# Optimization experiments

Measured on AMD Instinct MI355X. Metric: run time of the kernel, lower is better.

The kernel has to match this reference:

```python
import jax, jax.numpy as jnp
import numpy as np

JOINTS = 17
SKELETON = ((1, 2), (0, 1), (0, 2), (2, 4), (1, 3), (6, 8), (8, 10), (5, 7), (7, 9),
            (12, 14), (14, 16), (11, 13), (13, 15), (5, 6), (11, 12), (5, 11), (6, 12),
            (3, 5), (4, 6))
DIM = 512
HEADS = 8
HEAD_DIM = DIM // HEADS
SCALE = HEAD_DIM ** -0.5
ON = 64           # obj_emb seq len; HEADS*ON must equal 512 (size of W)
HIDDEN = 4 * DIM
BN_EPS = 1e-5
LN_EPS = 1e-5


def make_adj():
    a = np.eye(JOINTS, dtype=np.float32)
    for i, j in SKELETON:
        a[i, j] = 1.0
        a[j, i] = 1.0
    return jnp.asarray(a)


def layer_norm(x, w, b):
    mu = jnp.mean(x, axis=-1, keepdims=True)
    var = jnp.var(x, axis=-1, keepdims=True)
    return (x - mu) * jax.lax.rsqrt(var + LN_EPS) * w + b


def setup_inputs() -> dict:
    key = jax.random.key(0)
    ks = jax.random.split(key, 12)
    B = 2048
    inp = {
        "noise": jax.random.normal(ks[0], (B, JOINTS, DIM), jnp.float32),
        "obj_emb": jax.random.normal(ks[1], (B, ON, DIM), jnp.float32),
        "ln1_w": jnp.ones((DIM,), jnp.float32),
        "ln1_b": jnp.zeros((DIM,), jnp.float32),
        "ln2_w": jnp.ones((DIM,), jnp.float32),
        "ln2_b": jnp.zeros((DIM,), jnp.float32),
        "q_w": jax.random.normal(ks[2], (DIM, DIM), jnp.float32) * 0.02,
        "kv_w": jax.random.normal(ks[3], (2 * DIM, DIM), jnp.float32) * 0.02,
        "W": jax.random.normal(ks[4], (HEADS * ON, HEADS * ON), jnp.float32) * 0.001,
        "bn_g": jnp.ones((HEADS * ON,), jnp.float32),
        "bn_b": jnp.zeros((HEADS * ON,), jnp.float32),
        "proj_w": jax.random.normal(ks[5], (DIM, DIM), jnp.float32) * 0.02,
        "proj_b": jnp.zeros((DIM,), jnp.float32),
        "fc1_w": jax.random.normal(ks[6], (HIDDEN, DIM), jnp.float32) * 0.02,
        "fc1_b": jnp.zeros((HIDDEN,), jnp.float32),
        "fc2_w": jax.random.normal(ks[7], (DIM, HIDDEN), jnp.float32) * 0.02,
        "fc2_b": jnp.zeros((DIM,), jnp.float32),
    }
    return inp


def reference(noise, obj_emb, ln1_w, ln1_b, ln2_w, ln2_b, q_w, kv_w, W,
              bn_g, bn_b, proj_w, proj_b, fc1_w, fc1_b, fc2_w, fc2_b):
    B = noise.shape[0]
    adj = make_adj()

    # --- attention branch (norm1 applied to both inputs with same params) ---
    x1 = layer_norm(noise, ln1_w, ln1_b)          # [B,17,C]
    e1 = layer_norm(obj_emb, ln1_w, ln1_b)        # [B,64,C]

    q = (x1 @ q_w.T).reshape(B, JOINTS, HEADS, HEAD_DIM).transpose(0, 2, 1, 3)  # [B,H,17,hd]
    kv = (e1 @ kv_w.T).reshape(B, ON, 2, HEADS, HEAD_DIM).transpose(2, 0, 3, 1, 4)
    k, v = kv[0], kv[1]                            # [B,H,64,hd]

    attn = jnp.einsum('bhnd,bhmd->bhnm', q, k) * SCALE        # [B,H,17,64]
    attn = attn.transpose(0, 2, 1, 3).reshape(B, JOINTS, HEADS * ON)  # [B,17,512]
    attn = attn @ W                                            # [B,17,512]

    # BatchNorm1d (training mode): stats over B*17 rows, biased variance
    flat = attn.reshape(B * JOINTS, HEADS * ON)
    mu = jnp.mean(flat, axis=0)
    var = jnp.var(flat, axis=0)
    flat = (flat - mu) * jax.lax.rsqrt(var + BN_EPS) * bn_g + bn_b
    attn = flat.reshape(B, JOINTS, HEADS * ON)

    attn = jnp.einsum('ij,bjk->bik', adj, attn)               # adjacency bmm
    attn = attn.reshape(B, JOINTS, HEADS, ON).transpose(0, 2, 1, 3)  # [B,H,17,64]
    attn = jax.nn.softmax(attn, axis=-1)

    x = jnp.einsum('bhnm,bhmd->bhnd', attn, v)                # [B,H,17,hd]
    x = x.transpose(0, 2, 1, 3).reshape(B, JOINTS, DIM)
    x = x @ proj_w.T + proj_b

    x = noise + x

    # --- MLP branch ---
    y = layer_norm(x, ln2_w, ln2_b)
    y = jax.nn.gelu(y @ fc1_w.T + fc1_b, approximate=False)
    y = y @ fc2_w.T + fc2_b
    return x + y
```

## Files before the change

kernel.cpp:

```cpp
#include <hip/hip_runtime.h>
#include <math.h>

typedef unsigned short ushort_t;
typedef short short8 __attribute__((ext_vector_type(8)));
typedef float f32x4 __attribute__((ext_vector_type(4)));

#define MFMA16(a,b,c) __builtin_amdgcn_mfma_f32_16x16x32_bf16(a,b,c,0,0,0)

__device__ __forceinline__ ushort_t f2bf(float f){
  unsigned u = __builtin_bit_cast(unsigned, f);
  u += 0x7fffu + ((u >> 16) & 1u);
  return (ushort_t)(u >> 16);
}

__device__ __forceinline__ void gld16(const void* g, void* l){
  __builtin_amdgcn_global_load_lds(
      (const __attribute__((address_space(1))) void*)g,
      (__attribute__((address_space(3))) void*)l, 16, 0, 0);
}

__global__ __launch_bounds__(256)
void prep_weights(const float* __restrict__ q_w, const float* __restrict__ kv_w,
                  const float* __restrict__ proj_w, const float* __restrict__ fc1_w,
                  const float* __restrict__ fc2_w, const float* __restrict__ Wm,
                  const float* __restrict__ ln1w, const float* __restrict__ ln2w,
                  ushort_t* __restrict__ q_wb, ushort_t* __restrict__ kv_wb,
                  ushort_t* __restrict__ proj_wb, ushort_t* __restrict__ fc1_wb,
                  ushort_t* __restrict__ fc2_wb, ushort_t* __restrict__ Wt_b)
{
  int i = blockIdx.x*256 + threadIdx.x;
  if (i < 262144){
    q_wb[i] = f2bf(q_w[i] * ln1w[i & 511]);
  } else if (i < 786432){
    int j = i - 262144;
    kv_wb[j] = f2bf(kv_w[j] * ln1w[j & 511]);
  } else if (i < 1048576){
    int j = i - 786432;
    proj_wb[j] = f2bf(proj_w[j]);
  } else if (i < 2097152){
    int j = i - 1048576;
    fc1_wb[j] = f2bf(fc1_w[j] * ln2w[j & 511]);
  } else if (i < 3145728){
    int j = i - 2097152;
    fc2_wb[j] = f2bf(fc2_w[j]);
  } else if (i < 3407872){
    int j = i - 3145728;
    int n = j >> 9, k = j & 511;
    Wt_b[j] = f2bf(Wm[(k << 9) + n]);
  }
}

__global__ __launch_bounds__(64)
void prep_bias(const float* __restrict__ q_w, const float* __restrict__ kv_w,
               const float* __restrict__ fc1_w, const float* __restrict__ ln1b,
               const float* __restrict__ ln2b, const float* __restrict__ fc1_b,
               float* __restrict__ qbias, float* __restrict__ kvbias,
               float* __restrict__ fc1bias)
{
  int blk = blockIdx.x, lane = threadIdx.x;
  const float* w; const float* lnb; float* o; float base = 0.f; int n;
  if (blk < 512){ n = blk; w = q_w; lnb = ln1b; o = qbias; }
  else if (blk < 1536){ n = blk - 512; w = kv_w; lnb = ln1b; o = kvbias; }
  else { n = blk - 1536; w = fc1_w; lnb = ln2b; o = fc1bias; }
  float s = 0.f;
  for (int k = lane; k < 512; k += 64) s += w[(size_t)n*512 + k]*lnb[k];
  for (int m = 32; m; m >>= 1) s += __shfl_xor(s, m);
  if (lane == 0){
    if (blk >= 1536) base = fc1_b[n];
    o[n] = s + base;
  }
}

__global__ __launch_bounds__(256)
void lnorm(const float* __restrict__ X, ushort_t* __restrict__ O){
  int row = blockIdx.x*4 + (threadIdx.x >> 6);
  int lane = threadIdx.x & 63;
  const float4* p = (const float4*)(X + (size_t)row*512 + lane*8);
  float4 a = p[0], c = p[1];
  float s = a.x+a.y+a.z+a.w + c.x+c.y+c.z+c.w;
  float q = a.x*a.x+a.y*a.y+a.z*a.z+a.w*a.w + c.x*c.x+c.y*c.y+c.z*c.z+c.w*c.w;
  for (int m = 32; m; m >>= 1){ s += __shfl_xor(s, m); q += __shfl_xor(q, m); }
  float mn = s*(1.f/512.f);
  float rs = rsqrtf(q*(1.f/512.f) - mn*mn + 1e-5f);
  short8 pk;
  pk[0]=(short)f2bf((a.x-mn)*rs); pk[1]=(short)f2bf((a.y-mn)*rs);
  pk[2]=(short)f2bf((a.z-mn)*rs); pk[3]=(short)f2bf((a.w-mn)*rs);
  pk[4]=(short)f2bf((c.x-mn)*rs); pk[5]=(short)f2bf((c.y-mn)*rs);
  pk[6]=(short)f2bf((c.z-mn)*rs); pk[7]=(short)f2bf((c.w-mn)*rs);
  *(short8*)(O + (size_t)row*512 + lane*8) = pk;
}

template<int EPI>
__global__ __launch_bounds__(256, 3)
void gemm128(const ushort_t* __restrict__ A, const ushort_t* __restrict__ Bt,
             int M, int N, int K,
             const float* __restrict__ bias, const float* __restrict__ resid,
             void* __restrict__ out, void* __restrict__ out2)
{
  constexpr int ASLOT = 128*32;
  constexpr int SLOT  = 2*ASLOT;
  __shared__ __align__(16) ushort_t lds[3*SLOT];

  const int tid  = threadIdx.x;
  const int wave = tid >> 6, lane = tid & 63;
  const int wm   = wave >> 1, wn = wave & 1;
  const int l15  = lane & 15, lq = lane >> 4;

  const int nwg = gridDim.x;
  const int qc = nwg >> 3, rc = nwg & 7;
  const int xcd = blockIdx.x & 7, sl = blockIdx.x >> 3;
  const int bid = (xcd < rc ? xcd*(qc+1) : rc*(qc+1) + (xcd-rc)*qc) + sl;

  const int tiles_n = N >> 7;
  const int tn = bid % tiles_n, tm = bid / tiles_n;
  const int tileM = tm*128, tileN = tn*128;

  const int r0   = tid >> 2;
  const int r1   = (tid + 256) >> 2;
  const int g0   = (((tid & 3) - (r0 >> 1)) & 3) * 8;
  const int g1   = (((tid & 3) - (r1 >> 1)) & 3) * 8;
  const ushort_t* Ag0 = A  + (size_t)(tileM + r0)*K + g0;
  const ushort_t* Ag1 = A  + (size_t)(tileM + r1)*K + g1;
  const ushort_t* Bg0 = Bt + (size_t)(tileN + r0)*K + g0;
  const ushort_t* Bg1 = Bt + (size_t)(tileN + r1)*K + g1;

  auto stage = [&](int step, int slot){
    ushort_t* base = lds + slot*SLOT;
    const int k0 = step*32;
    gld16(Ag0 + k0, base + tid*8);
    gld16(Ag1 + k0, base + tid*8 + 2048);
    gld16(Bg0 + k0, base + ASLOT + tid*8);
    gld16(Bg1 + k0, base + ASLOT + tid*8 + 2048);
  };

  int offA[4], offB[4];
#pragma unroll
  for (int mi = 0; mi < 4; mi++){
    int r = wm*64 + mi*16 + l15;
    offA[mi] = r*32 + (((lq + (r >> 1)) & 3) * 8);
  }
#pragma unroll
  for (int ni = 0; ni < 4; ni++){
    int r = wn*64 + ni*16 + l15;
    offB[ni] = ASLOT + r*32 + (((lq + (r >> 1)) & 3) * 8);
  }

  f32x4 acc[4][4] = {};

  const int NT = K >> 5;

  stage(0, 0);
  stage(1, 1);
  asm volatile("s_waitcnt vmcnt(4)" ::: "memory");
  __builtin_amdgcn_sched_barrier(0);
  __builtin_amdgcn_s_barrier();
  __builtin_amdgcn_sched_barrier(0);

  int rs = 0;
  for (int s = 0; s < NT; ++s){
    const ushort_t* sb = lds + rs*SLOT;
    short8 aR[4], bR[4];
#pragma unroll
    for (int mi = 0; mi < 4; mi++) aR[mi] = *(const short8*)(sb + offA[mi]);
#pragma unroll
    for (int ni = 0; ni < 4; ni++) bR[ni] = *(const short8*)(sb + offB[ni]);

    const bool more = (s + 2 < NT);
    if (more){
      int r2 = rs + 2; if (r2 >= 3) r2 -= 3;
      stage(s + 2, r2);
    }

    __builtin_amdgcn_s_setprio(1);
#pragma unroll
    for (int mi = 0; mi < 4; mi++)
#pragma unroll
      for (int ni = 0; ni < 4; ni++)
        acc[mi][ni] = MFMA16(aR[mi], bR[ni], acc[mi][ni]);
    __builtin_amdgcn_s_setprio(0);

    if (more){
      asm volatile("s_waitcnt vmcnt(4)" ::: "memory");
    } else {
      asm volatile("s_waitcnt vmcnt(0)" ::: "memory");
    }
    __builtin_amdgcn_sched_barrier(0);
    __builtin_amdgcn_s_barrier();
    __builtin_amdgcn_sched_barrier(0);

    rs = (rs == 2) ? 0 : rs + 1;
  }

#pragma unroll
  for (int ni = 0; ni < 4; ni++){
    int col = tileN + wn*64 + ni*16 + l15;
    float bv = bias ? bias[col] : 0.f;
    float cs = 0.f, cq = 0.f;
#pragma unroll
    for (int mi = 0; mi < 4; mi++){
      f32x4 v = acc[mi][ni];
      int row0 = tileM + wm*64 + mi*16 + lq*4;
      if constexpr (EPI == 4){
        if (col < 512){
          for (int j = 0; j < 4; j++){
            size_t idx = (size_t)(row0 + j)*512 + col;
            ((ushort_t*)out)[idx] = f2bf(v[j] + bv);
          }
        } else {
          int hh = (col - 512) >> 6, dd = (col - 512) & 63;
          int bb2 = row0 >> 6, mm0 = row0 & 63;
          ushort_t pk[4];
          for (int j = 0; j < 4; j++) pk[j] = f2bf(v[j] + bv);
          *(uint2*)((ushort_t*)out2 + ((((size_t)bb2*8 + hh)*64 + dd) << 6) + mm0) =
              *(const uint2*)pk;
        }
      } else {
        for (int j = 0; j < 4; j++){
          int row = row0 + j;
          size_t idx = (size_t)row*N + col;
          float x = v[j] + bv;
          if constexpr (EPI == 0) ((ushort_t*)out)[idx] = f2bf(x);
          else if constexpr (EPI == 1) ((float*)out)[idx] = x;
          else if constexpr (EPI == 2) ((float*)out)[idx] = x + resid[idx];
          else if constexpr (EPI == 3){
            float g = 0.5f*x*(1.f + erff(x*0.70710678118f));
            ((ushort_t*)out)[idx] = f2bf(g);
          }
          else if constexpr (EPI == 5){
            ((float*)out)[idx] = x;
            cs += x; cq += x*x;
          }
        }
      }
    }
    if constexpr (EPI == 5){
      cs += __shfl_xor(cs, 16); cs += __shfl_xor(cs, 32);
      cq += __shfl_xor(cq, 16); cq += __shfl_xor(cq, 32);
      if (lq == 0){
        float* sums = (float*)out2;
        atomicAdd(&sums[col], cs);
        atomicAdd(&sums[512 + col], cq);
      }
    }
  }
}

__global__ __launch_bounds__(256)
void qk_kernel(const ushort_t* __restrict__ Q, const ushort_t* __restrict__ Kb,
               ushort_t* __restrict__ S)
{
  int b = blockIdx.x;
  int wave = threadIdx.x >> 6, lane = threadIdx.x & 63;
  for (int h = wave; h < 8; h += 4){
    f32x4 acc[2][4] = {};
    for (int kk = 0; kk < 2; kk++){
      int kd = kk*32 + (lane >> 4)*8;
      short8 a[2], bb[4];
      for (int mi = 0; mi < 2; mi++){
        int n = mi*16 + (lane & 15); if (n > 16) n = 16;
        a[mi] = *(const short8*)&Q[((size_t)b*17 + n)*512 + h*64 + kd];
      }
      for (int ni = 0; ni < 4; ni++){
        int m = ni*16 + (lane & 15);
        bb[ni] = *(const short8*)&Kb[((size_t)b*64 + m)*512 + h*64 + kd];
      }
      for (int mi = 0; mi < 2; mi++)
        for (int ni = 0; ni < 4; ni++)
          acc[mi][ni] = MFMA16(a[mi], bb[ni], acc[mi][ni]);
    }
    for (int mi = 0; mi < 2; mi++)
      for (int ni = 0; ni < 4; ni++)
        for (int j = 0; j < 4; j++){
          int rr = mi*16 + (lane >> 4)*4 + j;
          if (rr < 17)
            S[((size_t)b*17 + rr)*512 + h*64 + ni*16 + (lane & 15)] =
                f2bf(acc[mi][ni][j]*0.125f);
        }
  }
}

__global__ __launch_bounds__(256)
void pv_kernel(const ushort_t* __restrict__ P, const ushort_t* __restrict__ Vt,
               ushort_t* __restrict__ X)
{
  int b = blockIdx.x;
  int wave = threadIdx.x >> 6, lane = threadIdx.x & 63;
  for (int h = wave; h < 8; h += 4){
    f32x4 acc[2][4] = {};
    for (int kk = 0; kk < 2; kk++){
      int km = kk*32 + (lane >> 4)*8;
      short8 a[2], bb[4];
      for (int mi = 0; mi < 2; mi++){
        int n = mi*16 + (lane & 15); if (n > 16) n = 16;
        a[mi] = *(const short8*)&P[((size_t)b*17 + n)*512 + h*64 + km];
      }
      for (int ni = 0; ni < 4; ni++){
        int d = ni*16 + (lane & 15);
        bb[ni] = *(const short8*)&Vt[(((size_t)b*8 + h)*64 + d)*64 + km];
      }
      for (int mi = 0; mi < 2; mi++)
        for (int ni = 0; ni < 4; ni++)
          acc[mi][ni] = MFMA16(a[mi], bb[ni], acc[mi][ni]);
    }
    for (int mi = 0; mi < 2; mi++)
      for (int ni = 0; ni < 4; ni++)
        for (int j = 0; j < 4; j++){
          int rr = mi*16 + (lane >> 4)*4 + j;
          if (rr < 17)
            X[((size_t)b*17 + rr)*512 + h*64 + ni*16 + (lane & 15)] =
                f2bf(acc[mi][ni][j]);
        }
  }
}

__global__ void bn_finalize(const float* __restrict__ sums, const float* __restrict__ g,
                            const float* __restrict__ b, float* __restrict__ scale,
                            float* __restrict__ shift, float invN){
  int c = blockIdx.x*256 + threadIdx.x;
  if (c < 512){
    float mean = sums[c]*invN;
    float var  = sums[512 + c]*invN - mean*mean;
    float sc = g[c]*rsqrtf(var + 1e-5f);
    scale[c] = sc; shift[c] = b[c] - mean*sc;
  }
}

__constant__ unsigned ADJM[17] = {
  0x7u, 0xFu, 0x17u, 0x2Au, 0x54u, 0x8E8u, 0x1170u, 0x2A0u, 0x540u,
  0x280u, 0x500u, 0x3820u, 0x5840u, 0xA800u, 0x15000u, 0xA000u, 0x14000u };

__global__ __launch_bounds__(256)
void bn_adj_softmax(const float* __restrict__ preBN, const float* __restrict__ scale,
                    const float* __restrict__ shift, ushort_t* __restrict__ Asm)
{
  __shared__ float yt[17*512];
  int b = blockIdx.x, tid = threadIdx.x;
  const float* src = preBN + (size_t)b*17*512;
  for (int i = tid; i < 17*512; i += 256){
    int c = i & 511;
    yt[i] = src[i]*scale[c] + shift[c];
  }
  __syncthreads();
  int qw = tid >> 4, l16 = tid & 15;
  for (int g = qw; g < 136; g += 16){
    int n = g >> 3, h = g & 7;
    float z[4];
    unsigned msk = ADJM[n];
    for (int u = 0; u < 4; u++){
      int c = h*64 + l16 + u*16;
      float sv = 0.f;
      unsigned mm = msk;
      while (mm){ int j = __ffs(mm) - 1; mm &= mm - 1; sv += yt[j*512 + c]; }
      z[u] = sv;
    }
    float mx = fmaxf(fmaxf(z[0], z[1]), fmaxf(z[2], z[3]));
    for (int m = 8; m; m >>= 1) mx = fmaxf(mx, __shfl_xor(mx, m, 16));
    float e0 = expf(z[0]-mx), e1 = expf(z[1]-mx), e2 = expf(z[2]-mx), e3 = expf(z[3]-mx);
    float ss = e0 + e1 + e2 + e3;
    for (int m = 8; m; m >>= 1) ss += __shfl_xor(ss, m, 16);
    float inv = 1.f/ss;
    size_t ob = ((size_t)b*17 + n)*512 + h*64 + l16;
    Asm[ob]      = f2bf(e0*inv);
    Asm[ob + 16] = f2bf(e1*inv);
    Asm[ob + 32] = f2bf(e2*inv);
    Asm[ob + 48] = f2bf(e3*inv);
  }
}

extern "C" void kernel_launch(void* const* d_in, const int* in_sizes, int n_in,
                              void* d_out, int out_size, void* d_ws, size_t ws_size,
                              hipStream_t stream)
{
  const float* noise  = (const float*)d_in[0];
  const float* obj    = (const float*)d_in[1];
  const float* ln1w   = (const float*)d_in[2];
  const float* ln1b   = (const float*)d_in[3];
  const float* ln2w   = (const float*)d_in[4];
  const float* ln2b   = (const float*)d_in[5];
  const float* q_w    = (const float*)d_in[6];
  const float* kv_w   = (const float*)d_in[7];
  const float* Wm     = (const float*)d_in[8];
  const float* bn_g   = (const float*)d_in[9];
  const float* bn_b   = (const float*)d_in[10];
  const float* proj_w = (const float*)d_in[11];
  const float* proj_b = (const float*)d_in[12];
  const float* fc1_w  = (const float*)d_in[13];
  const float* fc1_b  = (const float*)d_in[14];
  const float* fc2_w  = (const float*)d_in[15];
  const float* fc2_b  = (const float*)d_in[16];

  const int B  = in_sizes[0] / (17*512);
  const int M  = B*17;
  const int MO = B*64;

  const size_t MiB = 1ull << 20;
  char* ws = (char*)d_ws;

  ushort_t* q_wb    = (ushort_t*)(ws + 0*MiB);
  ushort_t* kv_wb   = (ushort_t*)(ws + 1*MiB);
  ushort_t* proj_wb = (ushort_t*)(ws + 2*MiB);
  ushort_t* fc1_wb  = (ushort_t*)(ws + 3*MiB);
  ushort_t* fc2_wb  = (ushort_t*)(ws + 5*MiB);
  ushort_t* Wt_b    = (ushort_t*)(ws + 7*MiB);
  float* qbias   = (float*)(ws + 7*MiB + 600*1024);
  float* kvbias  = qbias + 1024;
  float* fc1bias = kvbias + 1024;
  float* bnsum   = fc1bias + 2048;
  float* bnscale = bnsum + 1024;
  float* bnshift = bnscale + 512;

  char* R1 = ws + 8*MiB;
  char* R2 = ws + 136*MiB;
  char* R3 = ws + 264*MiB;

  ushort_t* e1b  = (ushort_t*)R1;
  ushort_t* Kb   = (ushort_t*)R2;
  ushort_t* Vtb  = (ushort_t*)R3;
  ushort_t* x1b  = (ushort_t*)R1;
  ushort_t* Qb   = (ushort_t*)(R1 + 35*MiB);
  ushort_t* Sb   = (ushort_t*)(R1 + 70*MiB);
  ushort_t* Asm  = (ushort_t*)R1;
  ushort_t* PVo  = (ushort_t*)(R1 + 35*MiB);
  float*    preBN = (float*)R2;
  float*    xres  = (float*)R2;
  ushort_t* yb   = (ushort_t*)(R2 + 69*MiB);
  ushort_t* h1   = (ushort_t*)(R2 + 104*MiB);
  float*    outp = (float*)d_out;

  hipMemsetAsync(bnsum, 0, 1024*4, stream);
  prep_weights<<<dim3(3407872/256), 256, 0, stream>>>(
      q_w, kv_w, proj_w, fc1_w, fc2_w, Wm, ln1w, ln2w,
      q_wb, kv_wb, proj_wb, fc1_wb, fc2_wb, Wt_b);
  prep_bias<<<dim3(3584), 64, 0, stream>>>(
      q_w, kv_w, fc1_w, ln1b, ln2b, fc1_b, qbias, kvbias, fc1bias);

  lnorm<<<dim3(MO/4), 256, 0, stream>>>(obj, e1b);
  gemm128<4><<<dim3((MO/128)*(1024/128)), 256, 0, stream>>>(
      e1b, kv_wb, MO, 1024, 512, kvbias, nullptr, Kb, Vtb);
  lnorm<<<dim3(M/4), 256, 0, stream>>>(noise, x1b);
  gemm128<0><<<dim3((M/128)*(512/128)), 256, 0, stream>>>(
      x1b, q_wb, M, 512, 512, qbias, nullptr, Qb, nullptr);
  qk_kernel<<<dim3(B), 256, 0, stream>>>(Qb, Kb, Sb);
  gemm128<5><<<dim3((M/128)*(512/128)), 256, 0, stream>>>(
      Sb, Wt_b, M, 512, 512, nullptr, nullptr, preBN, bnsum);
  bn_finalize<<<dim3(2), 256, 0, stream>>>(bnsum, bn_g, bn_b, bnscale, bnshift, 1.f/(float)M);
  bn_adj_softmax<<<dim3(B), 256, 0, stream>>>(preBN, bnscale, bnshift, Asm);
  pv_kernel<<<dim3(B), 256, 0, stream>>>(Asm, Vtb, PVo);
  gemm128<2><<<dim3((M/128)*(512/128)), 256, 0, stream>>>(
      PVo, proj_wb, M, 512, 512, proj_b, noise, xres, nullptr);

  lnorm<<<dim3(M/4), 256, 0, stream>>>(xres, yb);
  gemm128<3><<<dim3((M/128)*(2048/128)), 256, 0, stream>>>(
      yb, fc1_wb, M, 2048, 512, fc1bias, nullptr, h1, nullptr);
  gemm128<2><<<dim3((M/128)*(512/128)), 256, 0, stream>>>(
      h1, fc2_wb, M, 512, 2048, fc2_b, xres, outp, nullptr);
}
```

Before: 873.1 us.

## Fuse BN/adjacency softmax with PV matmul; switch GEMM to double buffering

The softmax probabilities now stay in LDS and feed the PV MFMA within the same block, so the separate pv_kernel launch and the global round trip of the probability tensor go away. Separately, the bf16 GEMM drops from a three-slot pipeline with explicit vmcnt waits to a two-slot double buffer with __syncthreads, and the occupancy hint rises from 3 to 5 blocks per CU. The smaller LDS footprint permits more resident blocks, but the prefetch is only one stage deep and each iteration now waits on a full barrier, which can expose global-load latency. The fused kernel also uses more LDS per block (about 52 KB), which may reduce its occupancy.

```diff
diff --git a/kernel.cpp b/kernel.cpp
--- a/kernel.cpp
+++ b/kernel.cpp
@@ -91,7 +91,7 @@
 }
 
 template<int EPI>
-__global__ __launch_bounds__(256, 3)
+__global__ __launch_bounds__(256, 5)
 void gemm128(const ushort_t* __restrict__ A, const ushort_t* __restrict__ Bt,
              int M, int N, int K,
              const float* __restrict__ bias, const float* __restrict__ resid,
@@ -99,7 +99,7 @@
 {
   constexpr int ASLOT = 128*32;
   constexpr int SLOT  = 2*ASLOT;
-  __shared__ __align__(16) ushort_t lds[3*SLOT];
+  __shared__ __align__(16) ushort_t lds[2*SLOT];
 
   const int tid  = threadIdx.x;
   const int wave = tid >> 6, lane = tid & 63;
@@ -150,26 +150,16 @@
   const int NT = K >> 5;
 
   stage(0, 0);
-  stage(1, 1);
-  asm volatile("s_waitcnt vmcnt(4)" ::: "memory");
-  __builtin_amdgcn_sched_barrier(0);
-  __builtin_amdgcn_s_barrier();
-  __builtin_amdgcn_sched_barrier(0);
-
-  int rs = 0;
+  __syncthreads();
+
   for (int s = 0; s < NT; ++s){
-    const ushort_t* sb = lds + rs*SLOT;
+    if (s + 1 < NT) stage(s + 1, (s + 1) & 1);
+    const ushort_t* sb = lds + (s & 1)*SLOT;
     short8 aR[4], bR[4];
 #pragma unroll
     for (int mi = 0; mi < 4; mi++) aR[mi] = *(const short8*)(sb + offA[mi]);
 #pragma unroll
     for (int ni = 0; ni < 4; ni++) bR[ni] = *(const short8*)(sb + offB[ni]);
-
-    const bool more = (s + 2 < NT);
-    if (more){
-      int r2 = rs + 2; if (r2 >= 3) r2 -= 3;
-      stage(s + 2, r2);
-    }
 
     __builtin_amdgcn_s_setprio(1);
 #pragma unroll
@@ -179,16 +169,7 @@
         acc[mi][ni] = MFMA16(aR[mi], bR[ni], acc[mi][ni]);
     __builtin_amdgcn_s_setprio(0);
 
-    if (more){
-      asm volatile("s_waitcnt vmcnt(4)" ::: "memory");
-    } else {
-      asm volatile("s_waitcnt vmcnt(0)" ::: "memory");
-    }
-    __builtin_amdgcn_sched_barrier(0);
-    __builtin_amdgcn_s_barrier();
-    __builtin_amdgcn_sched_barrier(0);
-
-    rs = (rs == 2) ? 0 : rs + 1;
+    __syncthreads();
   }
 
 #pragma unroll
@@ -279,40 +260,6 @@
   }
 }
 
-__global__ __launch_bounds__(256)
-void pv_kernel(const ushort_t* __restrict__ P, const ushort_t* __restrict__ Vt,
-               ushort_t* __restrict__ X)
-{
-  int b = blockIdx.x;
-  int wave = threadIdx.x >> 6, lane = threadIdx.x & 63;
-  for (int h = wave; h < 8; h += 4){
-    f32x4 acc[2][4] = {};
-    for (int kk = 0; kk < 2; kk++){
-      int km = kk*32 + (lane >> 4)*8;
-      short8 a[2], bb[4];
-      for (int mi = 0; mi < 2; mi++){
-        int n = mi*16 + (lane & 15); if (n > 16) n = 16;
-        a[mi] = *(const short8*)&P[((size_t)b*17 + n)*512 + h*64 + km];
-      }
-      for (int ni = 0; ni < 4; ni++){
-        int d = ni*16 + (lane & 15);
-        bb[ni] = *(const short8*)&Vt[(((size_t)b*8 + h)*64 + d)*64 + km];
-      }
-      for (int mi = 0; mi < 2; mi++)
-        for (int ni = 0; ni < 4; ni++)
-          acc[mi][ni] = MFMA16(a[mi], bb[ni], acc[mi][ni]);
-    }
-    for (int mi = 0; mi < 2; mi++)
-      for (int ni = 0; ni < 4; ni++)
-        for (int j = 0; j < 4; j++){
-          int rr = mi*16 + (lane >> 4)*4 + j;
-          if (rr < 17)
-            X[((size_t)b*17 + rr)*512 + h*64 + ni*16 + (lane & 15)] =
-                f2bf(acc[mi][ni][j]);
-        }
-  }
-}
-
 __global__ void bn_finalize(const float* __restrict__ sums, const float* __restrict__ g,
                             const float* __restrict__ b, float* __restrict__ scale,
                             float* __restrict__ shift, float invN){
@@ -330,10 +277,12 @@
   0x280u, 0x500u, 0x3820u, 0x5840u, 0xA800u, 0x15000u, 0xA000u, 0x14000u };
 
 __global__ __launch_bounds__(256)
-void bn_adj_softmax(const float* __restrict__ preBN, const float* __restrict__ scale,
-                    const float* __restrict__ shift, ushort_t* __restrict__ Asm)
+void bnadj_softmax_pv(const float* __restrict__ preBN, const float* __restrict__ scale,
+                      const float* __restrict__ shift, const ushort_t* __restrict__ Vt,
+                      ushort_t* __restrict__ X)
 {
   __shared__ float yt[17*512];
+  __shared__ __align__(16) ushort_t pl[17*520];
   int b = blockIdx.x, tid = threadIdx.x;
   const float* src = preBN + (size_t)b*17*512;
   for (int i = tid; i < 17*512; i += 256){
@@ -359,11 +308,40 @@
     float ss = e0 + e1 + e2 + e3;
     for (int m = 8; m; m >>= 1) ss += __shfl_xor(ss, m, 16);
     float inv = 1.f/ss;
-    size_t ob = ((size_t)b*17 + n)*512 + h*64 + l16;
-    Asm[ob]      = f2bf(e0*inv);
-    Asm[ob + 16] = f2bf(e1*inv);
-    Asm[ob + 32] = f2bf(e2*inv);
-    Asm[ob + 48] = f2bf(e3*inv);
+    int ob = n*520 + h*64 + l16;
+    pl[ob]      = f2bf(e0*inv);
+    pl[ob + 16] = f2bf(e1*inv);
+    pl[ob + 32] = f2bf(e2*inv);
+    pl[ob + 48] = f2bf(e3*inv);
+  }
+  __syncthreads();
+
+  int wave = tid >> 6, lane = tid & 63;
+  for (int h = wave; h < 8; h += 4){
+    f32x4 acc[2][4] = {};
+    for (int kk = 0; kk < 2; kk++){
+      int km = kk*32 + (lane >> 4)*8;
+      short8 a[2], bb[4];
+      for (int mi = 0; mi < 2; mi++){
+        int n = mi*16 + (lane & 15); if (n > 16) n = 16;
+        a[mi] = *(const short8*)&pl[n*520 + h*64 + km];
+      }
+      for (int ni = 0; ni < 4; ni++){
+        int d = ni*16 + (lane & 15);
+        bb[ni] = *(const short8*)&Vt[(((size_t)b*8 + h)*64 + d)*64 + km];
+      }
+      for (int mi = 0; mi < 2; mi++)
+        for (int ni = 0; ni < 4; ni++)
+          acc[mi][ni] = MFMA16(a[mi], bb[ni], acc[mi][ni]);
+    }
+    for (int mi = 0; mi < 2; mi++)
+      for (int ni = 0; ni < 4; ni++)
+        for (int j = 0; j < 4; j++){
+          int rr = mi*16 + (lane >> 4)*4 + j;
+          if (rr < 17)
+            X[((size_t)b*17 + rr)*512 + h*64 + ni*16 + (lane & 15)] =
+                f2bf(acc[mi][ni][j]);
+        }
   }
 }
 
@@ -419,7 +397,6 @@
   ushort_t* x1b  = (ushort_t*)R1;
   ushort_t* Qb   = (ushort_t*)(R1 + 35*MiB);
   ushort_t* Sb   = (ushort_t*)(R1 + 70*MiB);
-  ushort_t* Asm  = (ushort_t*)R1;
   ushort_t* PVo  = (ushort_t*)(R1 + 35*MiB);
   float*    preBN = (float*)R2;
   float*    xres  = (float*)R2;
@@ -444,8 +421,7 @@
   gemm128<5><<<dim3((M/128)*(512/128)), 256, 0, stream>>>(
       Sb, Wt_b, M, 512, 512, nullptr, nullptr, preBN, bnsum);
   bn_finalize<<<dim3(2), 256, 0, stream>>>(bnsum, bn_g, bn_b, bnscale, bnshift, 1.f/(float)M);
-  bn_adj_softmax<<<dim3(B), 256, 0, stream>>>(preBN, bnscale, bnshift, Asm);
-  pv_kernel<<<dim3(B), 256, 0, stream>>>(Asm, Vtb, PVo);
+  bnadj_softmax_pv<<<dim3(B), 256, 0, stream>>>(preBN, bnscale, bnshift, Vtb, PVo);
   gemm128<2><<<dim3((M/128)*(512/128)), 256, 0, stream>>>(
       PVo, proj_wb, M, 512, 512, proj_b, noise, xres, nullptr);
 
```

Result: slower. 2.359 ms (+170.2%).

## Fuse BN finalize, adjacency softmax and PV; add 256-row GEMM for KV

Applied to the files above, without the earlier changes.

The BN finalize, BN+adjacency+softmax, and PV matmul kernels become one kernel. Each block now computes the BN scale and shift itself and keeps the softmax probabilities in LDS instead of writing them to global memory and reading them back. A new 256x128-tile, 512-thread GEMM with XCD-aware block remapping replaces the 128-tile GEMM for the KV projection. This saves two launches and a round trip of the probability tensor. The cost is more LDS per block in the fused kernel and a different occupancy profile for the KV GEMM.

```diff
diff --git a/kernel.cpp b/kernel.cpp
--- a/kernel.cpp
+++ b/kernel.cpp
@@ -88,6 +88,162 @@
   pk[4]=(short)f2bf((c.x-mn)*rs); pk[5]=(short)f2bf((c.y-mn)*rs);
   pk[6]=(short)f2bf((c.z-mn)*rs); pk[7]=(short)f2bf((c.w-mn)*rs);
   *(short8*)(O + (size_t)row*512 + lane*8) = pk;
+}
+
+template<int BN, int EPI>
+__global__ __launch_bounds__(512, 4)
+void gemm256(const ushort_t* __restrict__ A, const ushort_t* __restrict__ Bt,
+             int M, int N, int K,
+             const float* __restrict__ bias, const float* __restrict__ resid,
+             void* __restrict__ out, void* __restrict__ out2)
+{
+  constexpr int NR    = BN / 64;
+  constexpr int ASLOT = 256 * 32;
+  constexpr int BSLOT = BN * 32;
+  constexpr int SLOT  = ASLOT + BSLOT;
+  __shared__ __align__(16) ushort_t lds[3 * SLOT];
+
+  const int tid  = threadIdx.x;
+  const int wave = tid >> 6, lane = tid & 63;
+  const int wm   = wave >> 2, wn = wave & 3;
+  const int l15  = lane & 15, lq = lane >> 4;
+
+  const int nwg = gridDim.x;
+  const int qc = nwg >> 3, rc = nwg & 7;
+  const int xcd = blockIdx.x & 7, sl = blockIdx.x >> 3;
+  const int bid = (xcd < rc ? xcd*(qc+1) : rc*(qc+1) + (xcd-rc)*qc) + sl;
+
+  const int tiles_n = N / BN;
+  const int tn = bid % tiles_n, tm = bid / tiles_n;
+  const int tileM = tm * 256, tileN = tn * BN;
+
+  const int gsw = (((tid & 3) - ((tid >> 3) & 3)) & 3) * 8;
+  const int srow = tid >> 2;
+
+  int offA[8], offB[NR];
+#pragma unroll
+  for (int mi = 0; mi < 8; mi++){
+    int r = wm*128 + mi*16 + l15;
+    offA[mi] = r*32 + (((lq + (r >> 1)) & 3) * 8);
+  }
+#pragma unroll
+  for (int ni = 0; ni < NR; ni++){
+    int r = wn*(BN/4) + ni*16 + l15;
+    offB[ni] = ASLOT + r*32 + (((lq + (r >> 1)) & 3) * 8);
+  }
+
+  f32x4 acc[8][NR] = {};
+
+  const int NT = K >> 5;
+
+  auto stage = [&](int step, int slot){
+    ushort_t* base = lds + slot * SLOT;
+    const int k0 = step * 32 + gsw;
+#pragma unroll
+    for (int i = 0; i < 2; i++)
+      gld16(A + (size_t)(tileM + i*128 + srow)*K + k0,
+            base + i*4096 + wave*512);
+#pragma unroll
+    for (int i = 0; i < BN/128; i++)
+      gld16(Bt + (size_t)(tileN + i*128 + srow)*K + k0,
+            base + ASLOT + i*4096 + wave*512);
+  };
+
+  stage(0, 0);
+  stage(1, 1);
+  if constexpr (BN == 256) asm volatile("s_waitcnt vmcnt(4)" ::: "memory");
+  else                     asm volatile("s_waitcnt vmcnt(3)" ::: "memory");
+  __builtin_amdgcn_sched_barrier(0);
+  __builtin_amdgcn_s_barrier();
+
+  int rs = 0;
+  for (int s = 0; s < NT; ++s){
+    const ushort_t* sb = lds + rs * SLOT;
+    short8 bfr[NR];
+#pragma unroll
+    for (int ni = 0; ni < NR; ni++)
+      bfr[ni] = *(const short8*)(sb + offB[ni]);
+
+    const bool more = (s + 2 < NT);
+    if (more){
+      int r2 = rs + 2; if (r2 >= 3) r2 -= 3;
+      stage(s + 2, r2);
+    }
+
+    __builtin_amdgcn_s_setprio(1);
+#pragma unroll
+    for (int mi = 0; mi < 8; mi++){
+      short8 af = *(const short8*)(sb + offA[mi]);
+#pragma unroll
+      for (int ni = 0; ni < NR; ni++)
+        acc[mi][ni] = MFMA16(af, bfr[ni], acc[mi][ni]);
+    }
+    __builtin_amdgcn_s_setprio(0);
+
+    if (more){
+      if constexpr (BN == 256) asm volatile("s_waitcnt vmcnt(4)" ::: "memory");
+      else                     asm volatile("s_waitcnt vmcnt(3)" ::: "memory");
+    } else {
+      asm volatile("s_waitcnt vmcnt(0)" ::: "memory");
+    }
+    __builtin_amdgcn_sched_barrier(0);
+    __builtin_amdgcn_s_barrier();
+
+    rs = (rs == 2) ? 0 : rs + 1;
+  }
+
+#pragma unroll
+  for (int ni = 0; ni < NR; ni++){
+    int col = tileN + wn*(BN/4) + ni*16 + l15;
+    float bv = bias ? bias[col] : 0.f;
+    float cs = 0.f, cq = 0.f;
+#pragma unroll
+    for (int mi = 0; mi < 8; mi++){
+      f32x4 v = acc[mi][ni];
+      int row0 = tileM + wm*128 + mi*16 + lq*4;
+      if constexpr (EPI == 4){
+        if (col < 512){
+          for (int j = 0; j < 4; j++){
+            size_t idx = (size_t)(row0 + j)*512 + col;
+            ((ushort_t*)out)[idx] = f2bf(v[j] + bv);
+          }
+        } else {
+          int hh = (col - 512) >> 6, dd = (col - 512) & 63;
+          int bb2 = row0 >> 6, mm0 = row0 & 63;
+          ushort_t pk[4];
+          for (int j = 0; j < 4; j++) pk[j] = f2bf(v[j] + bv);
+          *(uint2*)((ushort_t*)out2 + ((((size_t)bb2*8 + hh)*64 + dd) << 6) + mm0) =
+              *(const uint2*)pk;
+        }
+      } else {
+        for (int j = 0; j < 4; j++){
+          int row = row0 + j;
+          size_t idx = (size_t)row*N + col;
+          float x = v[j] + bv;
+          if constexpr (EPI == 0) ((ushort_t*)out)[idx] = f2bf(x);
+          else if constexpr (EPI == 1) ((float*)out)[idx] = x;
+          else if constexpr (EPI == 2) ((float*)out)[idx] = x + resid[idx];
+          else if constexpr (EPI == 3){
+            float g = 0.5f*x*(1.f + erff(x*0.70710678118f));
+            ((ushort_t*)out)[idx] = f2bf(g);
+          }
+          else if constexpr (EPI == 5){
+            ((float*)out)[idx] = x;
+            cs += x; cq += x*x;
+          }
+        }
+      }
+    }
+    if constexpr (EPI == 5){
+      cs += __shfl_xor(cs, 16); cs += __shfl_xor(cs, 32);
+      cq += __shfl_xor(cq, 16); cq += __shfl_xor(cq, 32);
+      if (lq == 0){
+        float* sums = (float*)out2;
+        atomicAdd(&sums[col], cs);
+        atomicAdd(&sums[512 + col], cq);
+      }
+    }
+  }
 }
 
 template<int EPI>
@@ -279,66 +435,34 @@
   }
 }
 
-__global__ __launch_bounds__(256)
-void pv_kernel(const ushort_t* __restrict__ P, const ushort_t* __restrict__ Vt,
-               ushort_t* __restrict__ X)
-{
-  int b = blockIdx.x;
-  int wave = threadIdx.x >> 6, lane = threadIdx.x & 63;
-  for (int h = wave; h < 8; h += 4){
-    f32x4 acc[2][4] = {};
-    for (int kk = 0; kk < 2; kk++){
-      int km = kk*32 + (lane >> 4)*8;
-      short8 a[2], bb[4];
-      for (int mi = 0; mi < 2; mi++){
-        int n = mi*16 + (lane & 15); if (n > 16) n = 16;
-        a[mi] = *(const short8*)&P[((size_t)b*17 + n)*512 + h*64 + km];
-      }
-      for (int ni = 0; ni < 4; ni++){
-        int d = ni*16 + (lane & 15);
-        bb[ni] = *(const short8*)&Vt[(((size_t)b*8 + h)*64 + d)*64 + km];
-      }
-      for (int mi = 0; mi < 2; mi++)
-        for (int ni = 0; ni < 4; ni++)
-          acc[mi][ni] = MFMA16(a[mi], bb[ni], acc[mi][ni]);
-    }
-    for (int mi = 0; mi < 2; mi++)
-      for (int ni = 0; ni < 4; ni++)
-        for (int j = 0; j < 4; j++){
-          int rr = mi*16 + (lane >> 4)*4 + j;
-          if (rr < 17)
-            X[((size_t)b*17 + rr)*512 + h*64 + ni*16 + (lane & 15)] =
-                f2bf(acc[mi][ni][j]);
-        }
-  }
-}
-
-__global__ void bn_finalize(const float* __restrict__ sums, const float* __restrict__ g,
-                            const float* __restrict__ b, float* __restrict__ scale,
-                            float* __restrict__ shift, float invN){
-  int c = blockIdx.x*256 + threadIdx.x;
-  if (c < 512){
-    float mean = sums[c]*invN;
-    float var  = sums[512 + c]*invN - mean*mean;
-    float sc = g[c]*rsqrtf(var + 1e-5f);
-    scale[c] = sc; shift[c] = b[c] - mean*sc;
-  }
-}
-
 __constant__ unsigned ADJM[17] = {
   0x7u, 0xFu, 0x17u, 0x2Au, 0x54u, 0x8E8u, 0x1170u, 0x2A0u, 0x540u,
   0x280u, 0x500u, 0x3820u, 0x5840u, 0xA800u, 0x15000u, 0xA000u, 0x14000u };
 
 __global__ __launch_bounds__(256)
-void bn_adj_softmax(const float* __restrict__ preBN, const float* __restrict__ scale,
-                    const float* __restrict__ shift, ushort_t* __restrict__ Asm)
+void bnadj_softmax_pv(const float* __restrict__ preBN, const float* __restrict__ bnsum,
+                      const float* __restrict__ bn_g, const float* __restrict__ bn_b,
+                      float invN, const ushort_t* __restrict__ Vt,
+                      ushort_t* __restrict__ X)
 {
   __shared__ float yt[17*512];
+  __shared__ __align__(16) ushort_t pl[17*520];
   int b = blockIdx.x, tid = threadIdx.x;
+
+  float sc[2], sh[2];
+#pragma unroll
+  for (int j = 0; j < 2; j++){
+    int c = tid + j*256;
+    float mean = bnsum[c]*invN;
+    float var  = bnsum[512 + c]*invN - mean*mean;
+    float s = bn_g[c]*rsqrtf(var + 1e-5f);
+    sc[j] = s; sh[j] = bn_b[c] - mean*s;
+  }
+
   const float* src = preBN + (size_t)b*17*512;
-  for (int i = tid; i < 17*512; i += 256){
-    int c = i & 511;
-    yt[i] = src[i]*scale[c] + shift[c];
+  for (int k = 0; k < 34; k++){
+    int i = tid + k*256;
+    yt[i] = src[i]*sc[k & 1] + sh[k & 1];
   }
   __syncthreads();
   int qw = tid >> 4, l16 = tid & 15;
@@ -359,11 +483,40 @@
     float ss = e0 + e1 + e2 + e3;
     for (int m = 8; m; m >>= 1) ss += __shfl_xor(ss, m, 16);
     float inv = 1.f/ss;
-    size_t ob = ((size_t)b*17 + n)*512 + h*64 + l16;
-    Asm[ob]      = f2bf(e0*inv);
-    Asm[ob + 16] = f2bf(e1*inv);
-    Asm[ob + 32] = f2bf(e2*inv);
-    Asm[ob + 48] = f2bf(e3*inv);
+    int ob = n*520 + h*64 + l16;
+    pl[ob]      = f2bf(e0*inv);
+    pl[ob + 16] = f2bf(e1*inv);
+    pl[ob + 32] = f2bf(e2*inv);
+    pl[ob + 48] = f2bf(e3*inv);
+  }
+  __syncthreads();
+
+  int wave = tid >> 6, lane = tid & 63;
+  for (int h = wave; h < 8; h += 4){
+    f32x4 acc[2][4] = {};
+    for (int kk = 0; kk < 2; kk++){
+      int km = kk*32 + (lane >> 4)*8;
+      short8 a[2], bb[4];
+      for (int mi = 0; mi < 2; mi++){
+        int n = mi*16 + (lane & 15); if (n > 16) n = 16;
+        a[mi] = *(const short8*)&pl[n*520 + h*64 + km];
+      }
+      for (int ni = 0; ni < 4; ni++){
+        int d = ni*16 + (lane & 15);
+        bb[ni] = *(const short8*)&Vt[(((size_t)b*8 + h)*64 + d)*64 + km];
+      }
+      for (int mi = 0; mi < 2; mi++)
+        for (int ni = 0; ni < 4; ni++)
+          acc[mi][ni] = MFMA16(a[mi], bb[ni], acc[mi][ni]);
+    }
+    for (int mi = 0; mi < 2; mi++)
+      for (int ni = 0; ni < 4; ni++)
+        for (int j = 0; j < 4; j++){
+          int rr = mi*16 + (lane >> 4)*4 + j;
+          if (rr < 17)
+            X[((size_t)b*17 + rr)*512 + h*64 + ni*16 + (lane & 15)] =
+                f2bf(acc[mi][ni][j]);
+        }
   }
 }
 
@@ -406,8 +559,6 @@
   float* kvbias  = qbias + 1024;
   float* fc1bias = kvbias + 1024;
   float* bnsum   = fc1bias + 2048;
-  float* bnscale = bnsum + 1024;
-  float* bnshift = bnscale + 512;
 
   char* R1 = ws + 8*MiB;
   char* R2 = ws + 136*MiB;
@@ -419,7 +570,6 @@
   ushort_t* x1b  = (ushort_t*)R1;
   ushort_t* Qb   = (ushort_t*)(R1 + 35*MiB);
   ushort_t* Sb   = (ushort_t*)(R1 + 70*MiB);
-  ushort_t* Asm  = (ushort_t*)R1;
   ushort_t* PVo  = (ushort_t*)(R1 + 35*MiB);
   float*    preBN = (float*)R2;
   float*    xres  = (float*)R2;
@@ -435,7 +585,7 @@
       q_w, kv_w, fc1_w, ln1b, ln2b, fc1_b, qbias, kvbias, fc1bias);
 
   lnorm<<<dim3(MO/4), 256, 0, stream>>>(obj, e1b);
-  gemm128<4><<<dim3((MO/128)*(1024/128)), 256, 0, stream>>>(
+  gemm256<128,4><<<dim3((MO/256)*(1024/128)), 512, 0, stream>>>(
       e1b, kv_wb, MO, 1024, 512, kvbias, nullptr, Kb, Vtb);
   lnorm<<<dim3(M/4), 256, 0, stream>>>(noise, x1b);
   gemm128<0><<<dim3((M/128)*(512/128)), 256, 0, stream>>>(
@@ -443,9 +593,8 @@
   qk_kernel<<<dim3(B), 256, 0, stream>>>(Qb, Kb, Sb);
   gemm128<5><<<dim3((M/128)*(512/128)), 256, 0, stream>>>(
       Sb, Wt_b, M, 512, 512, nullptr, nullptr, preBN, bnsum);
-  bn_finalize<<<dim3(2), 256, 0, stream>>>(bnsum, bn_g, bn_b, bnscale, bnshift, 1.f/(float)M);
-  bn_adj_softmax<<<dim3(B), 256, 0, stream>>>(preBN, bnscale, bnshift, Asm);
-  pv_kernel<<<dim3(B), 256, 0, stream>>>(Asm, Vtb, PVo);
+  bnadj_softmax_pv<<<dim3(B), 256, 0, stream>>>(
+      preBN, bnsum, bn_g, bn_b, 1.f/(float)M, Vtb, PVo);
   gemm128<2><<<dim3((M/128)*(512/128)), 256, 0, stream>>>(
       PVo, proj_wb, M, 512, 512, proj_b, noise, xres, nullptr);
 
```

Result: faster. 799.0 us (-8.5%).
